# Kernel optimization log

Measured on AMD Instinct MI355X. Metric: run time of the kernel, lower is better.

The kernel has to match this reference:

```python
import jax, jax.numpy as jnp
import numpy as np

DIM = 768
H = 12
DH = DIM // H          # 64
ROPE_DIM = (DH // 6) * 6   # 60
HALF = (ROPE_DIM // 3) // 2  # 10 freqs per axis
THETA = 10000.0
EPS = 1e-6


def rmsnorm(x, w):
    xf = x.astype(jnp.float32)
    var = jnp.mean(xf * xf, axis=-1, keepdims=True)
    return (w * (xf * jax.lax.rsqrt(var + EPS))).astype(x.dtype)


def rope_angles(positions):
    # positions: [B, N, 3] -> angles [B, N, 3*HALF]
    freqs = 1.0 / (THETA ** (jnp.arange(HALF, dtype=jnp.float32) / HALF))  # [HALF]
    # [B,N,3,1] * [1,1,1,HALF] -> [B,N,3,HALF] -> concat over axis order x,y,z
    ang = positions[..., :, None] * freqs[None, None, None, :]
    return ang.reshape(*positions.shape[:2], 3 * HALF)  # [B,N,30]


def apply_rope(t, cos, sin):
    # t: [B,N,H,ROPE_DIM]; cos/sin: [B,N,1,ROPE_DIM//2]
    B, N, Hh, D = t.shape
    tf = t.astype(jnp.float32).reshape(B, N, Hh, D // 2, 2)
    te, to = tf[..., 0], tf[..., 1]
    oe = te * cos - to * sin
    oo = te * sin + to * cos
    return jnp.stack([oe, oo], axis=-1).reshape(B, N, Hh, D).astype(t.dtype)


def setup_inputs() -> dict:
    key = jax.random.key(0)
    ks = jax.random.split(key, 5)
    B, N = 2, 2048
    x = jax.random.normal(ks[0], (B, N, DIM), dtype=jnp.float32)
    positions = jax.random.uniform(ks[1], (B, N, 3), dtype=jnp.float32)
    qkv_w = jax.random.normal(ks[2], (3 * DIM, DIM), dtype=jnp.float32) * (DIM ** -0.5)
    proj_w = jax.random.normal(ks[3], (DIM, DIM), dtype=jnp.float32) * (DIM ** -0.5)
    proj_b = jnp.zeros((DIM,), dtype=jnp.float32)
    qn_w = jnp.ones((DH,), dtype=jnp.float32)
    kn_w = jnp.ones((DH,), dtype=jnp.float32)
    return {"x": x, "positions": positions, "qkv_w": qkv_w, "proj_w": proj_w,
            "proj_b": proj_b, "qn_w": qn_w, "kn_w": kn_w}


def reference(x, positions, qkv_w, proj_w, proj_b, qn_w, kn_w):
    B, N, C = x.shape
    scale = DH ** -0.5
    qkv = (x @ qkv_w.T).reshape(B, N, 3, H, DH)
    q, k, v = qkv[:, :, 0], qkv[:, :, 1], qkv[:, :, 2]  # [B,N,H,DH]
    q = rmsnorm(q, qn_w)
    k = rmsnorm(k, kn_w)
    # 3D RoPE on first ROPE_DIM channels
    ang = rope_angles(positions)                 # [B,N,30]
    cos = jnp.cos(ang)[:, :, None, :]            # [B,N,1,30]
    sin = jnp.sin(ang)[:, :, None, :]
    q = jnp.concatenate([apply_rope(q[..., :ROPE_DIM], cos, sin), q[..., ROPE_DIM:]], axis=-1)
    k = jnp.concatenate([apply_rope(k[..., :ROPE_DIM], cos, sin), k[..., ROPE_DIM:]], axis=-1)
    attn = jnp.einsum('bqhd,bkhd->bhqk', q, k) * scale  # [B,H,N,N]
    attn = jax.nn.softmax(attn, axis=-1)
    out = jnp.einsum('bhqk,bkhd->bqhd', attn, v).reshape(B, N, C)
    return out @ proj_w.T + proj_b
```

## Files before the change

kernel.cpp:

```cpp
#include <hip/hip_runtime.h>
#include <hip/hip_bf16.h>
#include <math.h>

#define DIM 768
#define NH 12
#define DH 64
#define SEQ 2048
#define BATCH 2
#define TOK (BATCH*SEQ)
#define QKVN (3*DIM)

typedef __attribute__((ext_vector_type(8))) short bf16x8;
typedef __attribute__((ext_vector_type(4))) float f32x4;
typedef __attribute__((ext_vector_type(2))) unsigned int u32x2;
typedef unsigned short u16;

#define VM0 asm volatile("s_waitcnt vmcnt(0)" ::: "memory")
#define VM4 asm volatile("s_waitcnt vmcnt(4)" ::: "memory")
#define LGKM0 asm volatile("s_waitcnt lgkmcnt(0)" ::: "memory")
#define BAR() __builtin_amdgcn_s_barrier()

__device__ inline u16 f2bf(float f) {
  union { float f; unsigned u; } v; v.f = f;
  unsigned u = v.u;
  u += 0x7fffu + ((u >> 16) & 1u);
  return (u16)(u >> 16);
}

__device__ inline int pkbf(float a, float b) {
  __hip_bfloat162 h = __float22bfloat162_rn(make_float2(a, b));
  int r; __builtin_memcpy(&r, &h, 4); return r;
}

__global__ void conv_all(const float* __restrict__ a, u16* __restrict__ ao, int na4,
                         const float* __restrict__ b, u16* __restrict__ bo, int nb4,
                         const float* __restrict__ c, u16* __restrict__ co, int nc4,
                         const float* __restrict__ pos, float2* __restrict__ tab) {
  int i4 = blockIdx.x * blockDim.x + threadIdx.x;
  const int nconv = na4 + nb4 + nc4;
  if (i4 < nconv) {
    const float* src; u16* dst; int off;
    if (i4 < na4)            { src = a; dst = ao; off = i4; }
    else if (i4 < na4 + nb4) { src = b; dst = bo; off = i4 - na4; }
    else                     { src = c; dst = co; off = i4 - na4 - nb4; }
    float4 v = ((const float4*)src)[off];
    ushort4 o;
    o.x = f2bf(v.x); o.y = f2bf(v.y); o.z = f2bf(v.z); o.w = f2bf(v.w);
    ((ushort4*)dst)[off] = o;
    return;
  }
  int e = i4 - nconv;
  if (e >= TOK * 32) return;
  int t = e >> 5, p = e & 31;
  float cs = 1.f, sn = 0.f;
  if (p < 30) {
    int axis = p / 10, fi = p % 10;
    float freq = exp2f(-(float)fi * 1.3287712379549449f);
    float ang = pos[t * 3 + axis] * freq;
    cs = cosf(ang); sn = sinf(ang);
  }
  tab[e] = make_float2(cs, sn);
}

#define GLL(g, s) __builtin_amdgcn_global_load_lds((const __attribute__((address_space(1))) void*)(g), (__attribute__((address_space(3))) void*)(s), 16, 0, 0)

__global__ __launch_bounds__(256, 4) void gemm64(
    const u16* __restrict__ A, const u16* __restrict__ W,
    float* __restrict__ C, const float* __restrict__ bias,
    int M, int Nn, int K)
{
  __shared__ u16 As[2][64 * 64];
  __shared__ u16 Bs[2][64 * 64];
  const int t = threadIdx.x;
  const int w = t >> 6, l = t & 63;
  const int lr = l & 15, lg = l >> 4;
  const int wr = w >> 1, wc = w & 1;
  const int m0 = blockIdx.x * 64;
  const int n0 = blockIdx.y * 64;
  f32x4 acc[2][2] = {};
  const int srow = t >> 3;
  const int scol = (((t & 7) ^ (srow & 7)) * 8);
  const u16* aSrc = A + (size_t)(m0 + srow) * K + scol;
  const u16* bSrc = W + (size_t)(n0 + srow) * K + scol;
  const size_t r32 = (size_t)32 * K;
  const int sw = lr & 7;
  const int NT = K / 64;

  GLL(aSrc,       &As[0][w * 512]);
  GLL(aSrc + r32, &As[0][2048 + w * 512]);
  GLL(bSrc,       &Bs[0][w * 512]);
  GLL(bSrc + r32, &Bs[0][2048 + w * 512]);

  for (int kt = 0; kt < NT; ++kt) {
    const int cur = kt & 1;
    if (kt + 1 < NT) {
      const int k0 = (kt + 1) * 64;
      GLL(aSrc + k0,       &As[cur ^ 1][w * 512]);
      GLL(aSrc + r32 + k0, &As[cur ^ 1][2048 + w * 512]);
      GLL(bSrc + k0,       &Bs[cur ^ 1][w * 512]);
      GLL(bSrc + r32 + k0, &Bs[cur ^ 1][2048 + w * 512]);
      VM4;
    } else {
      VM0;
    }
    BAR();
#pragma unroll
    for (int kk = 0; kk < 2; ++kk) {
      bf16x8 af[2], bff[2];
#pragma unroll
      for (int mi = 0; mi < 2; ++mi)
        af[mi] = *(const bf16x8*)(&As[cur][0] + (wr * 32 + mi * 16 + lr) * 64 + (((kk * 4 + lg) ^ sw) * 8));
#pragma unroll
      for (int ni = 0; ni < 2; ++ni)
        bff[ni] = *(const bf16x8*)(&Bs[cur][0] + (wc * 32 + ni * 16 + lr) * 64 + (((kk * 4 + lg) ^ sw) * 8));
#pragma unroll
      for (int mi = 0; mi < 2; ++mi)
#pragma unroll
        for (int ni = 0; ni < 2; ++ni)
          acc[mi][ni] = __builtin_amdgcn_mfma_f32_16x16x32_bf16(af[mi], bff[ni], acc[mi][ni], 0, 0, 0);
    }
    LGKM0;
    BAR();
  }

#pragma unroll
  for (int mi = 0; mi < 2; ++mi)
#pragma unroll
    for (int ni = 0; ni < 2; ++ni)
#pragma unroll
      for (int r = 0; r < 4; ++r) {
        int row = m0 + wr * 32 + mi * 16 + lg * 4 + r;
        int col = n0 + wc * 32 + ni * 16 + lr;
        C[(size_t)row * Nn + col] = acc[mi][ni][r] + bias[col];
      }
}

__global__ __launch_bounds__(512, 2) void gemm_qkv(
    const u16* __restrict__ A, const u16* __restrict__ W,
    const float* __restrict__ qn_w, const float* __restrict__ kn_w,
    const float2* __restrict__ tab,
    u16* __restrict__ Qb, u16* __restrict__ Kb, u16* __restrict__ Vtb)
{
  __shared__ u16 As[2][128 * 64];
  __shared__ u16 Bs[2][128 * 64];
  const int K = DIM;
  const int t = threadIdx.x;
  const int w = t >> 6, l = t & 63;
  const int lr = l & 15, lg = l >> 4;
  const int wr = w >> 1, wc = w & 1;
  const int m0 = blockIdx.x * 128;
  const int n0 = blockIdx.y * 128;
  f32x4 acc[2][4] = {};
  const int srow = t >> 3;
  const int scol = (((t & 7) ^ (srow & 7)) * 8);
  const u16* aSrc = A + (size_t)(m0 + srow) * K + scol;
  const u16* bSrc = W + (size_t)(n0 + srow) * K + scol;
  const size_t r64 = (size_t)64 * K;
  const int sw = lr & 7;
  const int NT = K / 64;

  GLL(aSrc,       &As[0][w * 512]);
  GLL(aSrc + r64, &As[0][4096 + w * 512]);
  GLL(bSrc,       &Bs[0][w * 512]);
  GLL(bSrc + r64, &Bs[0][4096 + w * 512]);

  for (int kt = 0; kt < NT; ++kt) {
    const int cur = kt & 1;
    if (kt + 1 < NT) {
      const int k0 = (kt + 1) * 64;
      GLL(aSrc + k0,       &As[cur ^ 1][w * 512]);
      GLL(aSrc + r64 + k0, &As[cur ^ 1][4096 + w * 512]);
      GLL(bSrc + k0,       &Bs[cur ^ 1][w * 512]);
      GLL(bSrc + r64 + k0, &Bs[cur ^ 1][4096 + w * 512]);
      VM4;
    } else {
      VM0;
    }
    BAR();
#pragma unroll
    for (int kk = 0; kk < 2; ++kk) {
      bf16x8 af[2], bff[4];
#pragma unroll
      for (int mi = 0; mi < 2; ++mi)
        af[mi] = *(const bf16x8*)(&As[cur][0] + (wr * 32 + mi * 16 + lr) * 64 + (((kk * 4 + lg) ^ sw) * 8));
#pragma unroll
      for (int ni = 0; ni < 4; ++ni)
        bff[ni] = *(const bf16x8*)(&Bs[cur][0] + (wc * 64 + ni * 16 + lr) * 64 + (((kk * 4 + lg) ^ sw) * 8));
#pragma unroll
      for (int mi = 0; mi < 2; ++mi)
#pragma unroll
        for (int ni = 0; ni < 4; ++ni)
          acc[mi][ni] = __builtin_amdgcn_mfma_f32_16x16x32_bf16(af[mi], bff[ni], acc[mi][ni], 0, 0, 0);
    }
    LGKM0;
    BAR();
  }

  const int chunk = (n0 >> 6) + wc;
  const int tt = chunk / 12;
  const int h  = chunk % 12;
  const int bB = m0 >> 11;
  const int bh = bB * NH + h;

  if (tt == 2) {
#pragma unroll
    for (int mi = 0; mi < 2; ++mi) {
      const int nbase = (m0 + wr * 32 + mi * 16 + lg * 4) & 2047;
#pragma unroll
      for (int ni = 0; ni < 4; ++ni) {
        const int d = ni * 16 + lr;
        ushort4 o;
        o.x = f2bf(acc[mi][ni][0]); o.y = f2bf(acc[mi][ni][1]);
        o.z = f2bf(acc[mi][ni][2]); o.w = f2bf(acc[mi][ni][3]);
        *(ushort4*)(Vtb + ((size_t)bh * DH + d) * SEQ + nbase) = o;
      }
    }
  } else {
    const float* wv = (tt == 0 ? qn_w : kn_w);
    const float qs = (tt == 0 ? 0.125f * 1.4426950408889634f : 1.f);
    float wgt[4];
#pragma unroll
    for (int ni = 0; ni < 4; ++ni) wgt[ni] = wv[ni * 16 + lr];
    u16* outp = (tt == 0 ? Qb : Kb) + (size_t)bh * SEQ * DH;
#pragma unroll
    for (int mi = 0; mi < 2; ++mi) {
#pragma unroll
      for (int r = 0; r < 4; ++r) {
        float ss = 0.f;
#pragma unroll
        for (int ni = 0; ni < 4; ++ni) ss += acc[mi][ni][r] * acc[mi][ni][r];
        ss += __shfl_xor(ss, 1, 64);
        ss += __shfl_xor(ss, 2, 64);
        ss += __shfl_xor(ss, 4, 64);
        ss += __shfl_xor(ss, 8, 64);
        const float rms = rsqrtf(ss * (1.f / 64.f) + 1e-6f);
        const int trow = m0 + wr * 32 + mi * 16 + lg * 4 + r;
        const float2* tl = tab + trow * 32;
        u16* rowp = outp + (size_t)(trow & 2047) * DH;
#pragma unroll
        for (int ni = 0; ni < 4; ++ni) {
          const int d = ni * 16 + lr;
          float v = acc[mi][ni][r] * rms * wgt[ni];
          float vp = __shfl_xor(v, 1, 64);
          float2 cssn = tl[ni * 8 + (lr >> 1)];
          float sgn = (d & 1) ? cssn.y : -cssn.y;
          rowp[d] = f2bf((v * cssn.x + vp * sgn) * qs);
        }
      }
    }
  }
}

__global__ __launch_bounds__(256, 3) void attn(
    const u16* __restrict__ Qb, const u16* __restrict__ Kb,
    const u16* __restrict__ Vtb, u16* __restrict__ Ob)
{
  __shared__ u16 Ks[2][2][64 * 64];
  __shared__ u16 Vs[2][64 * 64];
  const int tid = threadIdx.x;
  const int w = tid >> 6, l = tid & 63;
  const int lr = l & 15, lg = l >> 4;
  const int qg = w & 1, half = w >> 1;
  const int wg = blockIdx.x;
  const int swz = (wg & 7) * 96 + (wg >> 3);
  const int bh = swz >> 5;
  const int q0 = (swz & 31) * 64;
  const u16* Qp = Qb + (size_t)bh * SEQ * DH;
  const u16* Kp = Kb + (size_t)bh * SEQ * DH;
  const u16* Vp = Vtb + (size_t)bh * DH * SEQ;

  const int qrA = q0 + qg * 32 + lr;
  const bf16x8 bq0a = *(const bf16x8*)(Qp + (size_t)qrA * DH + 8 * lg);
  const bf16x8 bq1a = *(const bf16x8*)(Qp + (size_t)qrA * DH + 32 + 8 * lg);
  const bf16x8 bq0b = *(const bf16x8*)(Qp + (size_t)(qrA + 16) * DH + 8 * lg);
  const bf16x8 bq1b = *(const bf16x8*)(Qp + (size_t)(qrA + 16) * DH + 32 + 8 * lg);

  const int srow = tid >> 3;
  const int sc16 = (tid & 7) ^ (srow & 7);
  const u16* kSrc = Kp + (size_t)srow * DH + sc16 * 8;
  const u16* vSrc = Vp + (size_t)srow * SEQ + sc16 * 8;

  const int frow = (lr & 3) | ((lr & 4) << 1) | ((lr & 8) >> 1);
  const int ksw = frow & 7;
  const int vsw = lr & 7;

  bf16x8 vone;
#pragma unroll
  for (int j = 0; j < 8; ++j) vone[j] = (short)0x3F80;

  f32x4 oaccA[4] = {}, oaccB[4] = {};
  f32x4 laccA = {}, laccB = {};

  GLL(kSrc,          &Ks[0][0][w * 512]);
  GLL(kSrc + 2048,   &Ks[0][0][w * 512 + 2048]);
  GLL(kSrc + 4096,   &Ks[0][1][w * 512]);
  GLL(kSrc + 6144,   &Ks[0][1][w * 512 + 2048]);
  VM0;
  BAR();
  GLL(vSrc,              &Vs[0][w * 512]);
  GLL(vSrc + 65536,      &Vs[0][w * 512 + 2048]);
  GLL(vSrc + 64,         &Vs[1][w * 512]);
  GLL(vSrc + 64 + 65536, &Vs[1][w * 512 + 2048]);
  GLL(kSrc + 8192,   &Ks[1][0][w * 512]);
  GLL(kSrc + 10240,  &Ks[1][0][w * 512 + 2048]);
  GLL(kSrc + 12288,  &Ks[1][1][w * 512]);
  GLL(kSrc + 14336,  &Ks[1][1][w * 512 + 2048]);

  for (int i = 0; i < 16; ++i) {
    const int p = i & 1;
    const u16* Kt = &Ks[p][half][0];
    const u16* Vt = &Vs[half][0];

    f32x4 paccA[4] = {}, paccB[4] = {};
    __builtin_amdgcn_s_setprio(1);
#pragma unroll
    for (int c = 0; c < 4; ++c) {
      const int rbase = (16 * c + frow) * 64;
      bf16x8 ka = *(const bf16x8*)(Kt + rbase + ((lg ^ ksw) * 8));
      bf16x8 kb = *(const bf16x8*)(Kt + rbase + (((4 + lg) ^ ksw) * 8));
      paccA[c] = __builtin_amdgcn_mfma_f32_16x16x32_bf16(ka, bq0a, paccA[c], 0, 0, 0);
      paccA[c] = __builtin_amdgcn_mfma_f32_16x16x32_bf16(kb, bq1a, paccA[c], 0, 0, 0);
      paccB[c] = __builtin_amdgcn_mfma_f32_16x16x32_bf16(ka, bq0b, paccB[c], 0, 0, 0);
      paccB[c] = __builtin_amdgcn_mfma_f32_16x16x32_bf16(kb, bq1b, paccB[c], 0, 0, 0);
    }
    __builtin_amdgcn_s_setprio(0);

    union { unsigned d[4]; bf16x8 v; } puA[2], puB[2];
#pragma unroll
    for (int g = 0; g < 2; ++g) {
      const int clo = 2 * g, chi = 2 * g + 1;
      float eA[8], eB[8];
#pragma unroll
      for (int r = 0; r < 4; ++r) {
        eA[r]     = __builtin_amdgcn_exp2f(paccA[clo][r] - 12.f);
        eA[4 + r] = __builtin_amdgcn_exp2f(paccA[chi][r] - 12.f);
        eB[r]     = __builtin_amdgcn_exp2f(paccB[clo][r] - 12.f);
        eB[4 + r] = __builtin_amdgcn_exp2f(paccB[chi][r] - 12.f);
      }
      u32x2 a0 = __builtin_amdgcn_permlane32_swap((unsigned)pkbf(eA[0], eA[1]),
                                                  (unsigned)pkbf(eA[4], eA[5]), false, false);
      u32x2 a1 = __builtin_amdgcn_permlane32_swap((unsigned)pkbf(eA[2], eA[3]),
                                                  (unsigned)pkbf(eA[6], eA[7]), false, false);
      u32x2 b0 = __builtin_amdgcn_permlane32_swap((unsigned)pkbf(eB[0], eB[1]),
                                                  (unsigned)pkbf(eB[4], eB[5]), false, false);
      u32x2 b1 = __builtin_amdgcn_permlane32_swap((unsigned)pkbf(eB[2], eB[3]),
                                                  (unsigned)pkbf(eB[6], eB[7]), false, false);
      puA[g].d[0] = a0[0]; puA[g].d[1] = a1[0]; puA[g].d[2] = a0[1]; puA[g].d[3] = a1[1];
      puB[g].d[0] = b0[0]; puB[g].d[1] = b1[0]; puB[g].d[2] = b0[1]; puB[g].d[3] = b1[1];
    }

    VM0;
    BAR();

    __builtin_amdgcn_s_setprio(1);
#pragma unroll
    for (int g = 0; g < 2; ++g) {
#pragma unroll
      for (int dt = 0; dt < 4; ++dt) {
        bf16x8 va = *(const bf16x8*)(Vt + (16 * dt + lr) * 64 + (((4 * g + lg) ^ vsw) * 8));
        oaccA[dt] = __builtin_amdgcn_mfma_f32_16x16x32_bf16(va, puA[g].v, oaccA[dt], 0, 0, 0);
        oaccB[dt] = __builtin_amdgcn_mfma_f32_16x16x32_bf16(va, puB[g].v, oaccB[dt], 0, 0, 0);
      }
      laccA = __builtin_amdgcn_mfma_f32_16x16x32_bf16(vone, puA[g].v, laccA, 0, 0, 0);
      laccB = __builtin_amdgcn_mfma_f32_16x16x32_bf16(vone, puB[g].v, laccB, 0, 0, 0);
    }
    __builtin_amdgcn_s_setprio(0);

    LGKM0;
    BAR();

    if (i + 1 < 16) {
      const size_t vo = (size_t)(2 * i + 2) * 64;
      GLL(vSrc + vo,              &Vs[0][w * 512]);
      GLL(vSrc + vo + 65536,      &Vs[0][w * 512 + 2048]);
      GLL(vSrc + vo + 64,         &Vs[1][w * 512]);
      GLL(vSrc + vo + 64 + 65536, &Vs[1][w * 512 + 2048]);
    }
    if (i + 2 < 16) {
      const size_t ko = (size_t)(2 * i + 4) * 4096;
      GLL(kSrc + ko,        &Ks[p][0][w * 512]);
      GLL(kSrc + ko + 2048, &Ks[p][0][w * 512 + 2048]);
      GLL(kSrc + ko + 4096, &Ks[p][1][w * 512]);
      GLL(kSrc + ko + 6144, &Ks[p][1][w * 512 + 2048]);
    }
  }

  float* scr = (float*)&Ks[0][0][0];
  const int sidA = (qg * 2 + 0) * 64 + l;
  const int sidB = (qg * 2 + 1) * 64 + l;
  if (half == 1) {
#pragma unroll
    for (int dt = 0; dt < 4; ++dt)
#pragma unroll
      for (int r = 0; r < 4; ++r) {
        scr[sidA * 17 + dt * 4 + r] = oaccA[dt][r];
        scr[sidB * 17 + dt * 4 + r] = oaccB[dt][r];
      }
    scr[sidA * 17 + 16] = laccA[0];
    scr[sidB * 17 + 16] = laccB[0];
  }
  __syncthreads();
  if (half == 1) return;
#pragma unroll
  for (int dt = 0; dt < 4; ++dt)
#pragma unroll
    for (int r = 0; r < 4; ++r) {
      oaccA[dt][r] += scr[sidA * 17 + dt * 4 + r];
      oaccB[dt][r] += scr[sidB * 17 + dt * 4 + r];
    }
  const float invA = 1.f / (laccA[0] + scr[sidA * 17 + 16]);
  const float invB = 1.f / (laccB[0] + scr[sidB * 17 + 16]);

  const int b = bh / NH, h = bh % NH;
  const int qA = q0 + qg * 32 + lr;
  size_t obA = (size_t)(b * SEQ + qA) * DIM + h * DH + 4 * lg;
  size_t obB = (size_t)(b * SEQ + qA + 16) * DIM + h * DH + 4 * lg;
#pragma unroll
  for (int dt = 0; dt < 4; ++dt) {
    ushort4 oA, oB;
    oA.x = f2bf(oaccA[dt][0] * invA); oA.y = f2bf(oaccA[dt][1] * invA);
    oA.z = f2bf(oaccA[dt][2] * invA); oA.w = f2bf(oaccA[dt][3] * invA);
    oB.x = f2bf(oaccB[dt][0] * invB); oB.y = f2bf(oaccB[dt][1] * invB);
    oB.z = f2bf(oaccB[dt][2] * invB); oB.w = f2bf(oaccB[dt][3] * invB);
    *(ushort4*)(Ob + obA + 16 * dt) = oA;
    *(ushort4*)(Ob + obB + 16 * dt) = oB;
  }
}

extern "C" void kernel_launch(void* const* d_in, const int* in_sizes, int n_in,
                              void* d_out, int out_size, void* d_ws, size_t ws_size,
                              hipStream_t stream) {
  const float* x      = (const float*)d_in[0];
  const float* pos    = (const float*)d_in[1];
  const float* qkv_w  = (const float*)d_in[2];
  const float* proj_w = (const float*)d_in[3];
  const float* proj_b = (const float*)d_in[4];
  const float* qn_w   = (const float*)d_in[5];
  const float* kn_w   = (const float*)d_in[6];
  char* ws = (char*)d_ws;
  u16*    xb    = (u16*)(ws + 0);
  u16*    wqkv  = (u16*)(ws + 6291456);
  u16*    wproj = (u16*)(ws + 9830400);
  float2* tab   = (float2*)(ws + 11010048);
  u16*    Qb    = (u16*)(ws + 12058624);
  u16*    Kb    = (u16*)(ws + 18350080);
  u16*    Vtb   = (u16*)(ws + 24641536);
  u16*    Ob    = (u16*)(ws + 30932992);
  float* out = (float*)d_out;

  const int na4 = TOK * DIM / 4, nb4 = QKVN * DIM / 4, nc4 = DIM * DIM / 4;
  const int ntot = na4 + nb4 + nc4 + TOK * 32;
  conv_all<<<(ntot + 255) / 256, 256, 0, stream>>>(
      x, xb, na4, qkv_w, wqkv, nb4, proj_w, wproj, nc4, pos, tab);

  dim3 g1(TOK / 128, QKVN / 128);
  gemm_qkv<<<g1, 512, 0, stream>>>(xb, wqkv, qn_w, kn_w, tab, Qb, Kb, Vtb);

  attn<<<SEQ / 64 * BATCH * NH, 256, 0, stream>>>(Qb, Kb, Vtb, Ob);

  dim3 g3(TOK / 64, DIM / 64);
  gemm64<<<g3, 256, 0, stream>>>(Ob, wproj, out, proj_b, TOK, DIM, DIM);
}
```

Baseline: 89.89 us.

## Shrink QKV GEMM tile to 128x64 and relax attention V-load wait

The QKV projection kernel now computes a 128x64 output tile per block. Each of its 8 waves owns a 16-row strip over the full 64-column head chunk, and the grid doubles along N. This halves shared memory per block and raises the occupancy hint, so more blocks can be resident and the grid covers the GPU better, at the cost of less operand reuse per loaded tile. In the attention kernel, the wait before the PV phase now leaves up to four loads outstanding (the K prefetch) and the full drain moves after the PV MFMAs. This lets K loads overlap the PV compute.

```diff
diff --git a/kernel.cpp b/kernel.cpp
--- a/kernel.cpp
+++ b/kernel.cpp
@@ -16,6 +16,7 @@
 typedef unsigned short u16;
 
 #define VM0 asm volatile("s_waitcnt vmcnt(0)" ::: "memory")
+#define VM3 asm volatile("s_waitcnt vmcnt(3)" ::: "memory")
 #define VM4 asm volatile("s_waitcnt vmcnt(4)" ::: "memory")
 #define LGKM0 asm volatile("s_waitcnt lgkmcnt(0)" ::: "memory")
 #define BAR() __builtin_amdgcn_s_barrier()
@@ -135,22 +136,21 @@
       }
 }
 
-__global__ __launch_bounds__(512, 2) void gemm_qkv(
+__global__ __launch_bounds__(512, 6) void gemm_qkv(
     const u16* __restrict__ A, const u16* __restrict__ W,
     const float* __restrict__ qn_w, const float* __restrict__ kn_w,
     const float2* __restrict__ tab,
     u16* __restrict__ Qb, u16* __restrict__ Kb, u16* __restrict__ Vtb)
 {
   __shared__ u16 As[2][128 * 64];
-  __shared__ u16 Bs[2][128 * 64];
+  __shared__ u16 Bs[2][64 * 64];
   const int K = DIM;
   const int t = threadIdx.x;
   const int w = t >> 6, l = t & 63;
   const int lr = l & 15, lg = l >> 4;
-  const int wr = w >> 1, wc = w & 1;
   const int m0 = blockIdx.x * 128;
-  const int n0 = blockIdx.y * 128;
-  f32x4 acc[2][4] = {};
+  const int n0 = blockIdx.y * 64;
+  f32x4 acc[4] = {};
   const int srow = t >> 3;
   const int scol = (((t & 7) ^ (srow & 7)) * 8);
   const u16* aSrc = A + (size_t)(m0 + srow) * K + scol;
@@ -162,7 +162,6 @@
   GLL(aSrc,       &As[0][w * 512]);
   GLL(aSrc + r64, &As[0][4096 + w * 512]);
   GLL(bSrc,       &Bs[0][w * 512]);
-  GLL(bSrc + r64, &Bs[0][4096 + w * 512]);
 
   for (int kt = 0; kt < NT; ++kt) {
     const int cur = kt & 1;
@@ -171,49 +170,41 @@
       GLL(aSrc + k0,       &As[cur ^ 1][w * 512]);
       GLL(aSrc + r64 + k0, &As[cur ^ 1][4096 + w * 512]);
       GLL(bSrc + k0,       &Bs[cur ^ 1][w * 512]);
-      GLL(bSrc + r64 + k0, &Bs[cur ^ 1][4096 + w * 512]);
-      VM4;
+      VM3;
     } else {
       VM0;
     }
     BAR();
 #pragma unroll
     for (int kk = 0; kk < 2; ++kk) {
-      bf16x8 af[2], bff[4];
-#pragma unroll
-      for (int mi = 0; mi < 2; ++mi)
-        af[mi] = *(const bf16x8*)(&As[cur][0] + (wr * 32 + mi * 16 + lr) * 64 + (((kk * 4 + lg) ^ sw) * 8));
+      bf16x8 af = *(const bf16x8*)(&As[cur][0] + (w * 16 + lr) * 64 + (((kk * 4 + lg) ^ sw) * 8));
+      bf16x8 bff[4];
 #pragma unroll
       for (int ni = 0; ni < 4; ++ni)
-        bff[ni] = *(const bf16x8*)(&Bs[cur][0] + (wc * 64 + ni * 16 + lr) * 64 + (((kk * 4 + lg) ^ sw) * 8));
-#pragma unroll
-      for (int mi = 0; mi < 2; ++mi)
-#pragma unroll
-        for (int ni = 0; ni < 4; ++ni)
-          acc[mi][ni] = __builtin_amdgcn_mfma_f32_16x16x32_bf16(af[mi], bff[ni], acc[mi][ni], 0, 0, 0);
+        bff[ni] = *(const bf16x8*)(&Bs[cur][0] + (ni * 16 + lr) * 64 + (((kk * 4 + lg) ^ sw) * 8));
+#pragma unroll
+      for (int ni = 0; ni < 4; ++ni)
+        acc[ni] = __builtin_amdgcn_mfma_f32_16x16x32_bf16(af, bff[ni], acc[ni], 0, 0, 0);
     }
     LGKM0;
     BAR();
   }
 
-  const int chunk = (n0 >> 6) + wc;
+  const int chunk = n0 >> 6;
   const int tt = chunk / 12;
   const int h  = chunk % 12;
   const int bB = m0 >> 11;
   const int bh = bB * NH + h;
 
   if (tt == 2) {
-#pragma unroll
-    for (int mi = 0; mi < 2; ++mi) {
-      const int nbase = (m0 + wr * 32 + mi * 16 + lg * 4) & 2047;
-#pragma unroll
-      for (int ni = 0; ni < 4; ++ni) {
-        const int d = ni * 16 + lr;
-        ushort4 o;
-        o.x = f2bf(acc[mi][ni][0]); o.y = f2bf(acc[mi][ni][1]);
-        o.z = f2bf(acc[mi][ni][2]); o.w = f2bf(acc[mi][ni][3]);
-        *(ushort4*)(Vtb + ((size_t)bh * DH + d) * SEQ + nbase) = o;
-      }
+    const int nbase = (m0 + w * 16 + lg * 4) & 2047;
+#pragma unroll
+    for (int ni = 0; ni < 4; ++ni) {
+      const int d = ni * 16 + lr;
+      ushort4 o;
+      o.x = f2bf(acc[ni][0]); o.y = f2bf(acc[ni][1]);
+      o.z = f2bf(acc[ni][2]); o.w = f2bf(acc[ni][3]);
+      *(ushort4*)(Vtb + ((size_t)bh * DH + d) * SEQ + nbase) = o;
     }
   } else {
     const float* wv = (tt == 0 ? qn_w : kn_w);
@@ -223,29 +214,26 @@
     for (int ni = 0; ni < 4; ++ni) wgt[ni] = wv[ni * 16 + lr];
     u16* outp = (tt == 0 ? Qb : Kb) + (size_t)bh * SEQ * DH;
 #pragma unroll
-    for (int mi = 0; mi < 2; ++mi) {
-#pragma unroll
-      for (int r = 0; r < 4; ++r) {
-        float ss = 0.f;
-#pragma unroll
-        for (int ni = 0; ni < 4; ++ni) ss += acc[mi][ni][r] * acc[mi][ni][r];
-        ss += __shfl_xor(ss, 1, 64);
-        ss += __shfl_xor(ss, 2, 64);
-        ss += __shfl_xor(ss, 4, 64);
-        ss += __shfl_xor(ss, 8, 64);
-        const float rms = rsqrtf(ss * (1.f / 64.f) + 1e-6f);
-        const int trow = m0 + wr * 32 + mi * 16 + lg * 4 + r;
-        const float2* tl = tab + trow * 32;
-        u16* rowp = outp + (size_t)(trow & 2047) * DH;
-#pragma unroll
-        for (int ni = 0; ni < 4; ++ni) {
-          const int d = ni * 16 + lr;
-          float v = acc[mi][ni][r] * rms * wgt[ni];
-          float vp = __shfl_xor(v, 1, 64);
-          float2 cssn = tl[ni * 8 + (lr >> 1)];
-          float sgn = (d & 1) ? cssn.y : -cssn.y;
-          rowp[d] = f2bf((v * cssn.x + vp * sgn) * qs);
-        }
+    for (int r = 0; r < 4; ++r) {
+      float ss = 0.f;
+#pragma unroll
+      for (int ni = 0; ni < 4; ++ni) ss += acc[ni][r] * acc[ni][r];
+      ss += __shfl_xor(ss, 1, 64);
+      ss += __shfl_xor(ss, 2, 64);
+      ss += __shfl_xor(ss, 4, 64);
+      ss += __shfl_xor(ss, 8, 64);
+      const float rms = rsqrtf(ss * (1.f / 64.f) + 1e-6f);
+      const int trow = m0 + w * 16 + lg * 4 + r;
+      const float2* tl = tab + trow * 32;
+      u16* rowp = outp + (size_t)(trow & 2047) * DH;
+#pragma unroll
+      for (int ni = 0; ni < 4; ++ni) {
+        const int d = ni * 16 + lr;
+        float v = acc[ni][r] * rms * wgt[ni];
+        float vp = __shfl_xor(v, 1, 64);
+        float2 cssn = tl[ni * 8 + (lr >> 1)];
+        float sgn = (d & 1) ? cssn.y : -cssn.y;
+        rowp[d] = f2bf((v * cssn.x + vp * sgn) * qs);
       }
     }
   }
@@ -349,7 +337,7 @@
       puB[g].d[0] = b0[0]; puB[g].d[1] = b1[0]; puB[g].d[2] = b0[1]; puB[g].d[3] = b1[1];
     }
 
-    VM0;
+    if (i < 15) { VM4; } else { VM0; }
     BAR();
 
     __builtin_amdgcn_s_setprio(1);
@@ -367,6 +355,7 @@
     __builtin_amdgcn_s_setprio(0);
 
     LGKM0;
+    VM0;
     BAR();
 
     if (i + 1 < 16) {
@@ -453,7 +442,7 @@
   conv_all<<<(ntot + 255) / 256, 256, 0, stream>>>(
       x, xb, na4, qkv_w, wqkv, nb4, proj_w, wproj, nc4, pos, tab);
 
-  dim3 g1(TOK / 128, QKVN / 128);
+  dim3 g1(TOK / 128, QKVN / 64);
   gemm_qkv<<<g1, 512, 0, stream>>>(xb, wqkv, qn_w, kn_w, tab, Qb, Kb, Vtb);
 
   attn<<<SEQ / 64 * BATCH * NH, 256, 0, stream>>>(Qb, Kb, Vtb, Ob);
```

New measurement: 88.62 us. About the same (-1.4%).
